# Performance work log

Measured on AMD Instinct MI355X. Metric: run time of the kernel, lower is better.

The kernel has to match this reference:

```python
import jax, jax.numpy as jnp
import numpy as np

EPS = 1e-5
INV_SQRT2 = 0.7071067811865476

def _rmsnorm(x, w):
    rms = jnp.sqrt(jnp.sum(x * x, axis=-1) / x.shape[-1] + EPS)
    return x / rms[..., None] * w

def _gelu(x):
    # exact erf-based GELU as in the torch module
    return x * (1.0 + jax.scipy.special.erf(x * INV_SQRT2)) * 0.5

def setup_inputs() -> dict:
    key = jax.random.key(0)
    ks = jax.random.split(key, 8)
    B, S, D, DFF = 4, 2048, 1024, 4096
    s = 0.02  # realistic init scale keeps softmax non-degenerate
    return {
        "x": jax.random.normal(ks[0], (B, S, D), jnp.float32),
        "ln1": jax.random.uniform(ks[1], (D,), jnp.float32),
        "ln2": jax.random.uniform(ks[2], (D,), jnp.float32),
        "ffn1": jax.random.normal(ks[3], (DFF, D), jnp.float32) * s,
        "ffn2": jax.random.normal(ks[4], (D, DFF), jnp.float32) * s,
        "k_proj": jax.random.normal(ks[5], (D, D), jnp.float32) * s,
        "q_proj": jax.random.normal(ks[6], (D, D), jnp.float32) * s,
        "v_proj": jax.random.normal(ks[7], (D, D), jnp.float32) * s,
        "out_proj": jax.random.normal(jax.random.fold_in(key, 99), (D, D), jnp.float32) * s,
    }

def reference(x, ln1, ln2, ffn1, ffn2, k_proj, q_proj, v_proj, out_proj):
    S = x.shape[1]
    d_k = x.shape[-1]
    # --- attention branch (single-head, as in source) ---
    h = _rmsnorm(x, ln1)
    Q = h @ q_proj.T  # [B,S,D]
    K = h @ k_proj.T
    V = h @ v_proj.T
    scores = jnp.einsum('bqd,bkd->bqk', Q, K) / jnp.sqrt(jnp.float32(d_k))
    attn = jax.nn.softmax(scores, axis=-1)
    # source: softmax first, then zero out strict-upper (future) entries, renormalize
    causal = jnp.tril(jnp.ones((S, S), jnp.float32))
    attn = attn * causal
    attn = attn / jnp.sum(attn, axis=-1, keepdims=True)
    mh = jnp.einsum('bqk,bkd->bqd', attn, V) @ out_proj
    y = x + mh
    # --- FFN branch: NOTE source feeds RMSNorm2(x), not y ---
    h2 = _rmsnorm(x, ln2)
    ff = _gelu(h2 @ ffn1.T) @ ffn2.T
    return y + ff
```

## Files before the change

kernel.cpp:

```cpp
#include <hip/hip_runtime.h>
#include <math.h>

typedef __bf16 bf16_t;
typedef __bf16 bf16x8 __attribute__((ext_vector_type(8)));
typedef float f32x4 __attribute__((ext_vector_type(4)));

#define LDS16(g, l) __builtin_amdgcn_global_load_lds( \
    (__attribute__((address_space(1))) void*)(g),     \
    (__attribute__((address_space(3))) void*)(l), 16, 0, 0)

__global__ __launch_bounds__(256) void cvt_all_kernel(
    const float* __restrict__ qp, const float* __restrict__ kp,
    const float* __restrict__ vp, const float* __restrict__ f1,
    const float* __restrict__ f2, bf16_t* __restrict__ qkvb,
    bf16_t* __restrict__ f1b, bf16_t* __restrict__ f2b)
{
    size_t i = ((size_t)blockIdx.x * 256 + threadIdx.x) * 4;
    const float* src;
    bf16_t* dst;
    if (i < 3145728) {
        if (i < 1048576)      { src = qp + i;            dst = qkvb + i; }
        else if (i < 2097152) { src = kp + (i - 1048576); dst = qkvb + i; }
        else                  { src = vp + (i - 2097152); dst = qkvb + i; }
    } else if (i < 7340032) { src = f1 + (i - 3145728); dst = f1b + (i - 3145728); }
    else                    { src = f2 + (i - 7340032); dst = f2b + (i - 7340032); }
    float4 v = *(const float4*)src;
    dst[0] = (bf16_t)v.x; dst[1] = (bf16_t)v.y;
    dst[2] = (bf16_t)v.z; dst[3] = (bf16_t)v.w;
}

__global__ __launch_bounds__(256) void transpose_cvt_kernel(
    const float* __restrict__ in, bf16_t* __restrict__ out, int rows, int cols)
{
    __shared__ float tile[32][33];
    int c0 = blockIdx.x * 32, r0 = blockIdx.y * 32;
    int tx = threadIdx.x & 31, ty = threadIdx.x >> 5;
#pragma unroll
    for (int i = 0; i < 32; i += 8)
        tile[ty + i][tx] = in[(size_t)(r0 + ty + i) * cols + c0 + tx];
    __syncthreads();
#pragma unroll
    for (int i = 0; i < 32; i += 8)
        out[(size_t)(c0 + ty + i) * rows + r0 + tx] = (bf16_t)tile[tx][ty + i];
}

__global__ __launch_bounds__(256) void transpose_bf16(
    const bf16_t* __restrict__ in, bf16_t* __restrict__ out,
    int rows, int ldin, long long sIn, long long sOut)
{
    __shared__ bf16_t tile[32][33];
    int b = blockIdx.z;
    const bf16_t* ip = in + (long long)b * sIn;
    bf16_t* op = out + (long long)b * sOut;
    int c0 = blockIdx.x * 32, r0 = blockIdx.y * 32;
    int tx = threadIdx.x & 31, ty = threadIdx.x >> 5;
#pragma unroll
    for (int i = 0; i < 32; i += 8)
        tile[ty + i][tx] = ip[(size_t)(r0 + ty + i) * ldin + c0 + tx];
    __syncthreads();
#pragma unroll
    for (int i = 0; i < 32; i += 8)
        op[(size_t)(c0 + ty + i) * rows + r0 + tx] = tile[tx][ty + i];
}

__global__ __launch_bounds__(256) void rmsnorm_kernel(
    const float* __restrict__ x, const float* __restrict__ w,
    bf16_t* __restrict__ h)
{
    int row = blockIdx.x;
    int t = threadIdx.x;
    float4 xv = ((const float4*)(x + (size_t)row * 1024))[t];
    float ss = xv.x * xv.x + xv.y * xv.y + xv.z * xv.z + xv.w * xv.w;
#pragma unroll
    for (int o = 32; o > 0; o >>= 1) ss += __shfl_xor(ss, o, 64);
    __shared__ float red[4];
    if ((t & 63) == 0) red[t >> 6] = ss;
    __syncthreads();
    ss = red[0] + red[1] + red[2] + red[3];
    float rinv = rsqrtf(ss * (1.0f / 1024.0f) + 1e-5f);
    float4 wv = ((const float4*)w)[t];
    bf16_t* hp = h + (size_t)row * 1024 + t * 4;
    hp[0] = (bf16_t)(xv.x * rinv * wv.x);
    hp[1] = (bf16_t)(xv.y * rinv * wv.y);
    hp[2] = (bf16_t)(xv.z * rinv * wv.z);
    hp[3] = (bf16_t)(xv.w * rinv * wv.w);
}

__global__ __launch_bounds__(256) void causal_softmax_kernel(bf16_t* __restrict__ SP)
{
    const int S = 2048;
    int q = blockIdx.x, b = blockIdx.y;
    bf16_t* row = SP + ((size_t)b * S + q) * S;
    int t = threadIdx.x;
    float v[8];
    float mx = -1e30f;
#pragma unroll
    for (int i = 0; i < 8; i++) {
        int j = i * 256 + t;
        v[i] = (j <= q) ? (float)row[j] : -1e30f;
        mx = fmaxf(mx, v[i]);
    }
#pragma unroll
    for (int o = 32; o > 0; o >>= 1) mx = fmaxf(mx, __shfl_xor(mx, o, 64));
    __shared__ float sm[4];
    if ((t & 63) == 0) sm[t >> 6] = mx;
    __syncthreads();
    mx = fmaxf(fmaxf(sm[0], sm[1]), fmaxf(sm[2], sm[3]));
    float e[8];
    float sum = 0.f;
#pragma unroll
    for (int i = 0; i < 8; i++) {
        e[i] = (v[i] > -1e29f) ? expf(v[i] - mx) : 0.f;
        sum += e[i];
    }
#pragma unroll
    for (int o = 32; o > 0; o >>= 1) sum += __shfl_xor(sum, o, 64);
    __shared__ float ssum[4];
    if ((t & 63) == 0) ssum[t >> 6] = sum;
    __syncthreads();
    sum = ssum[0] + ssum[1] + ssum[2] + ssum[3];
    float r = 1.0f / sum;
#pragma unroll
    for (int i = 0; i < 8; i++)
        row[i * 256 + t] = (bf16_t)(e[i] * r);
}

template <int EPI, bool CSKIP, bool CKLOOP>
__global__ __launch_bounds__(256) void gemm_bt(
    const bf16_t* __restrict__ A, int lda, const bf16_t* __restrict__ B, int ldb,
    void* Cv, int ldc, const float* R,
    int K, int Mt, long long sA, long long sB, long long sC, float scale)
{
    int id = blockIdx.x, bz = blockIdx.z;
    int xcd = id & 7, p = id >> 3;
    int chunk = Mt >> 3;
    int bm = xcd * chunk + (p % chunk);
    int bn = p / chunk;
    if (CSKIP && bn > bm) return;

    __shared__ __align__(16) bf16_t At[128 * 32];
    __shared__ __align__(16) bf16_t Bt[128 * 32];
    int t = threadIdx.x;
    int w = t >> 6, l = t & 63;
    int wm = w >> 1, wn = w & 1;
    int lane_m = l & 15, quad = l >> 4;

    const bf16_t* Ag = A + (long long)bz * sA + (size_t)(bm * 128) * lda;
    const bf16_t* Bg = B + (long long)bz * sB + (size_t)(bn * 128) * ldb;

    int Keff = K;
    if (CKLOOP) {
        int kk = (bm + 1) * 128;
        if (kk < K) Keff = kk;
    }

    f32x4 acc[4][4] = {};

    int r0 = w * 16 + (l >> 2);
    int g0 = ((l & 3) ^ ((l >> 3) & 3)) * 8;
    int r1 = r0 + 64;
    const bf16_t* a0 = Ag + (size_t)r0 * lda + g0;
    const bf16_t* a1 = Ag + (size_t)r1 * lda + g0;
    const bf16_t* b0 = Bg + (size_t)r0 * ldb + g0;
    const bf16_t* b1 = Bg + (size_t)r1 * ldb + g0;

    int sa = (quad ^ ((lane_m >> 1) & 3)) * 8;

    for (int kt = 0; kt < Keff; kt += 32) {
        __syncthreads();
        LDS16(a0 + kt, At + (size_t)w * 512);
        LDS16(a1 + kt, At + (size_t)(4 + w) * 512);
        LDS16(b0 + kt, Bt + (size_t)w * 512);
        LDS16(b1 + kt, Bt + (size_t)(4 + w) * 512);
        __syncthreads();

        bf16x8 af[4], bfr[4];
#pragma unroll
        for (int mi = 0; mi < 4; mi++)
            af[mi] = *(const bf16x8*)(At + (wm * 64 + mi * 16 + lane_m) * 32 + sa);
#pragma unroll
        for (int ni = 0; ni < 4; ni++)
            bfr[ni] = *(const bf16x8*)(Bt + (wn * 64 + ni * 16 + lane_m) * 32 + sa);
#pragma unroll
        for (int mi = 0; mi < 4; mi++)
#pragma unroll
            for (int ni = 0; ni < 4; ni++)
                acc[mi][ni] = __builtin_amdgcn_mfma_f32_16x16x32_bf16(
                    af[mi], bfr[ni], acc[mi][ni], 0, 0, 0);
    }

    long long cbase = (long long)bz * sC;
#pragma unroll
    for (int mi = 0; mi < 4; mi++) {
#pragma unroll
        for (int r = 0; r < 4; r++) {
            int row = bm * 128 + wm * 64 + mi * 16 + quad * 4 + r;
#pragma unroll
            for (int ni = 0; ni < 4; ni++) {
                int col = bn * 128 + wn * 64 + ni * 16 + lane_m;
                float v = acc[mi][ni][r];
                size_t idx = (size_t)(cbase + (long long)row * ldc + col);
                if (EPI == 0) {
                    ((bf16_t*)Cv)[idx] = (bf16_t)(v * scale);
                } else if (EPI == 1) {
                    float g = 0.5f * v * (1.0f + erff(v * 0.70710678118654752f));
                    ((bf16_t*)Cv)[idx] = (bf16_t)g;
                } else {
                    float rv = R[(size_t)row * ldc + col];
                    ((float*)Cv)[idx] = v + rv;
                }
            }
        }
    }
}

extern "C" void kernel_launch(void* const* d_in, const int* in_sizes, int n_in,
                              void* d_out, int out_size, void* d_ws, size_t ws_size,
                              hipStream_t stream)
{
    (void)in_sizes; (void)n_in; (void)out_size; (void)ws_size;
    const float* x    = (const float*)d_in[0];
    const float* ln1  = (const float*)d_in[1];
    const float* ln2  = (const float*)d_in[2];
    const float* ffn1 = (const float*)d_in[3];
    const float* ffn2 = (const float*)d_in[4];
    const float* kp   = (const float*)d_in[5];
    const float* qp   = (const float*)d_in[6];
    const float* vp   = (const float*)d_in[7];
    const float* op   = (const float*)d_in[8];
    float* out = (float*)d_out;

    const size_t MiB = 1048576;
    char* ws = (char*)d_ws;
    bf16_t* qkvb = (bf16_t*)(ws + 0 * MiB);
    bf16_t* opT  = (bf16_t*)(ws + 6 * MiB);
    bf16_t* f1b  = (bf16_t*)(ws + 8 * MiB);
    bf16_t* f2b  = (bf16_t*)(ws + 16 * MiB);
    bf16_t* h1   = (bf16_t*)(ws + 24 * MiB);
    bf16_t* VT   = (bf16_t*)(ws + 24 * MiB);
    bf16_t* h2   = (bf16_t*)(ws + 24 * MiB);
    bf16_t* QKVb = (bf16_t*)(ws + 40 * MiB);
    bf16_t* AV   = (bf16_t*)(ws + 40 * MiB);
    bf16_t* G    = (bf16_t*)(ws + 40 * MiB);
    bf16_t* SP   = (bf16_t*)d_out;

    dim3 blk(256);

    cvt_all_kernel<<<dim3(11264), blk, 0, stream>>>(
        qp, kp, vp, ffn1, ffn2, qkvb, f1b, f2b);
    transpose_cvt_kernel<<<dim3(32, 32), blk, 0, stream>>>(op, opT, 1024, 1024);

    rmsnorm_kernel<<<dim3(8192), blk, 0, stream>>>(x, ln1, h1);

    gemm_bt<0, false, false><<<dim3(1536), blk, 0, stream>>>(
        h1, 1024, qkvb, 1024, QKVb, 3072, nullptr, 1024, 64, 0, 0, 0, 1.0f);

    gemm_bt<0, true, false><<<dim3(256, 1, 4), blk, 0, stream>>>(
        QKVb, 3072, QKVb + 1024, 3072, SP, 2048, nullptr, 1024, 16,
        (long long)2048 * 3072, (long long)2048 * 3072, (long long)2048 * 2048,
        1.0f / 32.0f);

    transpose_bf16<<<dim3(32, 64, 4), blk, 0, stream>>>(
        QKVb + 2048, VT, 2048, 3072, (long long)2048 * 3072, (long long)1024 * 2048);

    causal_softmax_kernel<<<dim3(2048, 4), blk, 0, stream>>>(SP);

    gemm_bt<0, false, true><<<dim3(128, 1, 4), blk, 0, stream>>>(
        SP, 2048, VT, 2048, AV, 1024, nullptr, 2048, 16,
        (long long)2048 * 2048, (long long)1024 * 2048, (long long)2048 * 1024,
        1.0f);

    gemm_bt<2, false, false><<<dim3(512), blk, 0, stream>>>(
        AV, 1024, opT, 1024, out, 1024, x, 1024, 64, 0, 0, 0, 1.0f);

    rmsnorm_kernel<<<dim3(8192), blk, 0, stream>>>(x, ln2, h2);

    for (int half = 0; half < 2; half++) {
        gemm_bt<1, false, false><<<dim3(1024), blk, 0, stream>>>(
            h2, 1024, f1b + (size_t)half * 2048 * 1024, 1024, G, 2048, nullptr,
            1024, 64, 0, 0, 0, 1.0f);
        gemm_bt<2, false, false><<<dim3(512), blk, 0, stream>>>(
            G, 2048, f2b + half * 2048, 4096, out, 1024, out,
            2048, 64, 0, 0, 0, 1.0f);
    }
}
```

Before: 636.5 us.

## Double GEMM K-tile, fuse prep kernels, vectorize softmax, split-A FFN2 GEMM

The GEMM K step grows from 32 to 64, with a wider XOR swizzle. This halves the number of barrier pairs per K, at the cost of doubling LDS usage per block. The weight conversion, out_proj transpose and first RMSNorm are merged into one prep kernel to cut launch count. Causal softmax now uses 8-element vector loads and stores and only writes the columns up to the 128-aligned causal bound. When the workspace is big enough, the FFN runs as two FFN1 GEMMs plus a single FFN2 GEMM with K=4096 reading from two buffers, which avoids a second read-modify-write pass over the output.

After: 544.0 us. 1.17x faster.

```diff
diff --git a/kernel.cpp b/kernel.cpp
--- a/kernel.cpp
+++ b/kernel.cpp
@@ -9,58 +9,60 @@
     (__attribute__((address_space(1))) void*)(g),     \
     (__attribute__((address_space(3))) void*)(l), 16, 0, 0)
 
-__global__ __launch_bounds__(256) void cvt_all_kernel(
+__global__ __launch_bounds__(256) void prep_kernel(
     const float* __restrict__ qp, const float* __restrict__ kp,
     const float* __restrict__ vp, const float* __restrict__ f1,
-    const float* __restrict__ f2, bf16_t* __restrict__ qkvb,
-    bf16_t* __restrict__ f1b, bf16_t* __restrict__ f2b)
-{
-    size_t i = ((size_t)blockIdx.x * 256 + threadIdx.x) * 4;
-    const float* src;
-    bf16_t* dst;
-    if (i < 3145728) {
-        if (i < 1048576)      { src = qp + i;            dst = qkvb + i; }
-        else if (i < 2097152) { src = kp + (i - 1048576); dst = qkvb + i; }
-        else                  { src = vp + (i - 2097152); dst = qkvb + i; }
-    } else if (i < 7340032) { src = f1 + (i - 3145728); dst = f1b + (i - 3145728); }
-    else                    { src = f2 + (i - 7340032); dst = f2b + (i - 7340032); }
-    float4 v = *(const float4*)src;
-    dst[0] = (bf16_t)v.x; dst[1] = (bf16_t)v.y;
-    dst[2] = (bf16_t)v.z; dst[3] = (bf16_t)v.w;
-}
-
-__global__ __launch_bounds__(256) void transpose_cvt_kernel(
-    const float* __restrict__ in, bf16_t* __restrict__ out, int rows, int cols)
+    const float* __restrict__ f2, const float* __restrict__ op,
+    const float* __restrict__ x, const float* __restrict__ ln1,
+    bf16_t* __restrict__ qkvb, bf16_t* __restrict__ f1b,
+    bf16_t* __restrict__ f2b, bf16_t* __restrict__ opT,
+    bf16_t* __restrict__ h1)
 {
     __shared__ float tile[32][33];
-    int c0 = blockIdx.x * 32, r0 = blockIdx.y * 32;
-    int tx = threadIdx.x & 31, ty = threadIdx.x >> 5;
-#pragma unroll
-    for (int i = 0; i < 32; i += 8)
-        tile[ty + i][tx] = in[(size_t)(r0 + ty + i) * cols + c0 + tx];
-    __syncthreads();
-#pragma unroll
-    for (int i = 0; i < 32; i += 8)
-        out[(size_t)(c0 + ty + i) * rows + r0 + tx] = (bf16_t)tile[tx][ty + i];
-}
-
-__global__ __launch_bounds__(256) void transpose_bf16(
-    const bf16_t* __restrict__ in, bf16_t* __restrict__ out,
-    int rows, int ldin, long long sIn, long long sOut)
-{
-    __shared__ bf16_t tile[32][33];
-    int b = blockIdx.z;
-    const bf16_t* ip = in + (long long)b * sIn;
-    bf16_t* op = out + (long long)b * sOut;
-    int c0 = blockIdx.x * 32, r0 = blockIdx.y * 32;
-    int tx = threadIdx.x & 31, ty = threadIdx.x >> 5;
-#pragma unroll
-    for (int i = 0; i < 32; i += 8)
-        tile[ty + i][tx] = ip[(size_t)(r0 + ty + i) * ldin + c0 + tx];
-    __syncthreads();
-#pragma unroll
-    for (int i = 0; i < 32; i += 8)
-        op[(size_t)(c0 + ty + i) * rows + r0 + tx] = tile[tx][ty + i];
+    __shared__ float red[4];
+    int bid = blockIdx.x;
+    int t = threadIdx.x;
+    if (bid < 11264) {
+        size_t i = ((size_t)bid * 256 + t) * 4;
+        const float* src;
+        bf16_t* dst;
+        if (i < 3145728) {
+            if (i < 1048576)      { src = qp + i;             dst = qkvb + i; }
+            else if (i < 2097152) { src = kp + (i - 1048576); dst = qkvb + i; }
+            else                  { src = vp + (i - 2097152); dst = qkvb + i; }
+        } else if (i < 7340032) { src = f1 + (i - 3145728); dst = f1b + (i - 3145728); }
+        else                    { src = f2 + (i - 7340032); dst = f2b + (i - 7340032); }
+        float4 v = *(const float4*)src;
+        dst[0] = (bf16_t)v.x; dst[1] = (bf16_t)v.y;
+        dst[2] = (bf16_t)v.z; dst[3] = (bf16_t)v.w;
+    } else if (bid < 12288) {
+        int b2 = bid - 11264;
+        int c0 = (b2 & 31) * 32, r0 = (b2 >> 5) * 32;
+        int tx = t & 31, ty = t >> 5;
+#pragma unroll
+        for (int i = 0; i < 32; i += 8)
+            tile[ty + i][tx] = op[(size_t)(r0 + ty + i) * 1024 + c0 + tx];
+        __syncthreads();
+#pragma unroll
+        for (int i = 0; i < 32; i += 8)
+            opT[(size_t)(c0 + ty + i) * 1024 + r0 + tx] = (bf16_t)tile[tx][ty + i];
+    } else {
+        int row = bid - 12288;
+        float4 xv = ((const float4*)(x + (size_t)row * 1024))[t];
+        float ss = xv.x * xv.x + xv.y * xv.y + xv.z * xv.z + xv.w * xv.w;
+#pragma unroll
+        for (int o = 32; o > 0; o >>= 1) ss += __shfl_xor(ss, o, 64);
+        if ((t & 63) == 0) red[t >> 6] = ss;
+        __syncthreads();
+        ss = red[0] + red[1] + red[2] + red[3];
+        float rinv = rsqrtf(ss * (1.0f / 1024.0f) + 1e-5f);
+        float4 wv = ((const float4*)ln1)[t];
+        bf16_t* hp = h1 + (size_t)row * 1024 + t * 4;
+        hp[0] = (bf16_t)(xv.x * rinv * wv.x);
+        hp[1] = (bf16_t)(xv.y * rinv * wv.y);
+        hp[2] = (bf16_t)(xv.z * rinv * wv.z);
+        hp[3] = (bf16_t)(xv.w * rinv * wv.w);
+    }
 }
 
 __global__ __launch_bounds__(256) void rmsnorm_kernel(
@@ -86,26 +88,58 @@
     hp[3] = (bf16_t)(xv.w * rinv * wv.w);
 }
 
+__global__ __launch_bounds__(256) void transpose_bf16(
+    const bf16_t* __restrict__ in, bf16_t* __restrict__ out,
+    int rows, int ldin, long long sIn, long long sOut)
+{
+    __shared__ bf16_t tile[32][33];
+    int b = blockIdx.z;
+    const bf16_t* ip = in + (long long)b * sIn;
+    bf16_t* op = out + (long long)b * sOut;
+    int c0 = blockIdx.x * 32, r0 = blockIdx.y * 32;
+    int tx = threadIdx.x & 31, ty = threadIdx.x >> 5;
+#pragma unroll
+    for (int i = 0; i < 32; i += 8)
+        tile[ty + i][tx] = ip[(size_t)(r0 + ty + i) * ldin + c0 + tx];
+    __syncthreads();
+#pragma unroll
+    for (int i = 0; i < 32; i += 8)
+        op[(size_t)(c0 + ty + i) * rows + r0 + tx] = tile[tx][ty + i];
+}
+
 __global__ __launch_bounds__(256) void causal_softmax_kernel(bf16_t* __restrict__ SP)
 {
     const int S = 2048;
     int q = blockIdx.x, b = blockIdx.y;
     bf16_t* row = SP + ((size_t)b * S + q) * S;
     int t = threadIdx.x;
+    int j0 = t * 8;
+    int Jstore = ((q >> 7) + 1) << 7;
+
     float v[8];
-    float mx = -1e30f;
-#pragma unroll
-    for (int i = 0; i < 8; i++) {
-        int j = i * 256 + t;
-        v[i] = (j <= q) ? (float)row[j] : -1e30f;
-        mx = fmaxf(mx, v[i]);
-    }
+    if (j0 + 7 <= q) {
+        bf16x8 xv = *(const bf16x8*)(row + j0);
+#pragma unroll
+        for (int i = 0; i < 8; i++) v[i] = (float)xv[i];
+    } else if (j0 <= q) {
+#pragma unroll
+        for (int i = 0; i < 8; i++)
+            v[i] = (j0 + i <= q) ? (float)row[j0 + i] : -1e30f;
+    } else {
+#pragma unroll
+        for (int i = 0; i < 8; i++) v[i] = -1e30f;
+    }
+
+    float mx = v[0];
+#pragma unroll
+    for (int i = 1; i < 8; i++) mx = fmaxf(mx, v[i]);
 #pragma unroll
     for (int o = 32; o > 0; o >>= 1) mx = fmaxf(mx, __shfl_xor(mx, o, 64));
-    __shared__ float sm[4];
+    __shared__ float sm[4], ssum[4];
     if ((t & 63) == 0) sm[t >> 6] = mx;
     __syncthreads();
     mx = fmaxf(fmaxf(sm[0], sm[1]), fmaxf(sm[2], sm[3]));
+
     float e[8];
     float sum = 0.f;
 #pragma unroll
@@ -115,21 +149,26 @@
     }
 #pragma unroll
     for (int o = 32; o > 0; o >>= 1) sum += __shfl_xor(sum, o, 64);
-    __shared__ float ssum[4];
     if ((t & 63) == 0) ssum[t >> 6] = sum;
     __syncthreads();
     sum = ssum[0] + ssum[1] + ssum[2] + ssum[3];
     float r = 1.0f / sum;
-#pragma unroll
-    for (int i = 0; i < 8; i++)
-        row[i * 256 + t] = (bf16_t)(e[i] * r);
-}
-
-template <int EPI, bool CSKIP, bool CKLOOP>
+
+    if (j0 < Jstore) {
+        bf16x8 ov;
+#pragma unroll
+        for (int i = 0; i < 8; i++) ov[i] = (bf16_t)(e[i] * r);
+        *(bf16x8*)(row + j0) = ov;
+    }
+}
+
+template <int EPI, bool CSKIP, bool CKLOOP, bool ASPLIT>
 __global__ __launch_bounds__(256) void gemm_bt(
-    const bf16_t* __restrict__ A, int lda, const bf16_t* __restrict__ B, int ldb,
+    const bf16_t* __restrict__ A, const bf16_t* __restrict__ A2, int lda,
+    const bf16_t* __restrict__ B, int ldb,
     void* Cv, int ldc, const float* R,
-    int K, int Mt, long long sA, long long sB, long long sC, float scale)
+    int K, int Ksp, int Mt, long long sA, long long sB, long long sC,
+    float scale)
 {
     int id = blockIdx.x, bz = blockIdx.z;
     int xcd = id & 7, p = id >> 3;
@@ -138,8 +177,8 @@
     int bn = p / chunk;
     if (CSKIP && bn > bm) return;
 
-    __shared__ __align__(16) bf16_t At[128 * 32];
-    __shared__ __align__(16) bf16_t Bt[128 * 32];
+    __shared__ __align__(16) bf16_t At[128 * 64];
+    __shared__ __align__(16) bf16_t Bt[128 * 64];
     int t = threadIdx.x;
     int w = t >> 6, l = t & 63;
     int wm = w >> 1, wn = w & 1;
@@ -156,37 +195,51 @@
 
     f32x4 acc[4][4] = {};
 
-    int r0 = w * 16 + (l >> 2);
-    int g0 = ((l & 3) ^ ((l >> 3) & 3)) * 8;
-    int r1 = r0 + 64;
-    const bf16_t* a0 = Ag + (size_t)r0 * lda + g0;
-    const bf16_t* a1 = Ag + (size_t)r1 * lda + g0;
-    const bf16_t* b0 = Bg + (size_t)r0 * ldb + g0;
-    const bf16_t* b1 = Bg + (size_t)r1 * ldb + g0;
-
-    int sa = (quad ^ ((lane_m >> 1) & 3)) * 8;
-
-    for (int kt = 0; kt < Keff; kt += 32) {
+    int rb = w * 8 + (l >> 3);
+    int g0 = ((l & 7) ^ ((l >> 3) & 7)) * 8;
+    const bf16_t* a0[4];
+    const bf16_t* a1[4];
+    const bf16_t* b0[4];
+#pragma unroll
+    for (int j = 0; j < 4; j++) {
+        size_t ro = (size_t)(rb + 32 * j);
+        a0[j] = Ag + ro * lda + g0;
+        if (ASPLIT) a1[j] = A2 + (long long)bz * sA + (size_t)(bm * 128) * lda
+                           + ro * lda + g0;
+        b0[j] = Bg + ro * ldb + g0;
+    }
+
+    int s0 = (quad ^ (lane_m & 7)) * 8;
+    int s1 = ((4 + quad) ^ (lane_m & 7)) * 8;
+
+    for (int kt = 0; kt < Keff; kt += 64) {
         __syncthreads();
-        LDS16(a0 + kt, At + (size_t)w * 512);
-        LDS16(a1 + kt, At + (size_t)(4 + w) * 512);
-        LDS16(b0 + kt, Bt + (size_t)w * 512);
-        LDS16(b1 + kt, Bt + (size_t)(4 + w) * 512);
+#pragma unroll
+        for (int j = 0; j < 4; j++) {
+            const bf16_t* pa = a0[j] + kt;
+            if (ASPLIT && kt >= Ksp) pa = a1[j] + (kt - Ksp);
+            LDS16(pa, At + (size_t)w * 512 + j * 2048);
+            LDS16(b0[j] + kt, Bt + (size_t)w * 512 + j * 2048);
+        }
         __syncthreads();
 
-        bf16x8 af[4], bfr[4];
-#pragma unroll
-        for (int mi = 0; mi < 4; mi++)
-            af[mi] = *(const bf16x8*)(At + (wm * 64 + mi * 16 + lane_m) * 32 + sa);
-#pragma unroll
-        for (int ni = 0; ni < 4; ni++)
-            bfr[ni] = *(const bf16x8*)(Bt + (wn * 64 + ni * 16 + lane_m) * 32 + sa);
-#pragma unroll
-        for (int mi = 0; mi < 4; mi++)
+#pragma unroll
+        for (int h = 0; h < 2; h++) {
+            int sh = h ? s1 : s0;
+            bf16x8 af[4], bfr[4];
+#pragma unroll
+            for (int mi = 0; mi < 4; mi++)
+                af[mi] = *(const bf16x8*)(At + (wm * 64 + mi * 16 + lane_m) * 64 + sh);
 #pragma unroll
             for (int ni = 0; ni < 4; ni++)
-                acc[mi][ni] = __builtin_amdgcn_mfma_f32_16x16x32_bf16(
-                    af[mi], bfr[ni], acc[mi][ni], 0, 0, 0);
+                bfr[ni] = *(const bf16x8*)(Bt + (wn * 64 + ni * 16 + lane_m) * 64 + sh);
+#pragma unroll
+            for (int mi = 0; mi < 4; mi++)
+#pragma unroll
+                for (int ni = 0; ni < 4; ni++)
+                    acc[mi][ni] = __builtin_amdgcn_mfma_f32_16x16x32_bf16(
+                        af[mi], bfr[ni], acc[mi][ni], 0, 0, 0);
+        }
     }
 
     long long cbase = (long long)bz * sC;
@@ -218,7 +271,7 @@
                               void* d_out, int out_size, void* d_ws, size_t ws_size,
                               hipStream_t stream)
 {
-    (void)in_sizes; (void)n_in; (void)out_size; (void)ws_size;
+    (void)in_sizes; (void)n_in; (void)out_size;
     const float* x    = (const float*)d_in[0];
     const float* ln1  = (const float*)d_in[1];
     const float* ln2  = (const float*)d_in[2];
@@ -241,46 +294,63 @@
     bf16_t* h2   = (bf16_t*)(ws + 24 * MiB);
     bf16_t* QKVb = (bf16_t*)(ws + 40 * MiB);
     bf16_t* AV   = (bf16_t*)(ws + 40 * MiB);
-    bf16_t* G    = (bf16_t*)(ws + 40 * MiB);
+    bf16_t* G0   = (bf16_t*)(ws + 40 * MiB);
+    bf16_t* G1   = (bf16_t*)(ws + 72 * MiB);
     bf16_t* SP   = (bf16_t*)d_out;
+    bool bigws = ws_size >= 104 * MiB;
 
     dim3 blk(256);
-
-    cvt_all_kernel<<<dim3(11264), blk, 0, stream>>>(
-        qp, kp, vp, ffn1, ffn2, qkvb, f1b, f2b);
-    transpose_cvt_kernel<<<dim3(32, 32), blk, 0, stream>>>(op, opT, 1024, 1024);
-
-    rmsnorm_kernel<<<dim3(8192), blk, 0, stream>>>(x, ln1, h1);
-
-    gemm_bt<0, false, false><<<dim3(1536), blk, 0, stream>>>(
-        h1, 1024, qkvb, 1024, QKVb, 3072, nullptr, 1024, 64, 0, 0, 0, 1.0f);
-
-    gemm_bt<0, true, false><<<dim3(256, 1, 4), blk, 0, stream>>>(
-        QKVb, 3072, QKVb + 1024, 3072, SP, 2048, nullptr, 1024, 16,
+    const int HUGE_K = 1 << 30;
+
+    prep_kernel<<<dim3(20480), blk, 0, stream>>>(
+        qp, kp, vp, ffn1, ffn2, op, x, ln1, qkvb, f1b, f2b, opT, h1);
+
+    gemm_bt<0, false, false, false><<<dim3(1536), blk, 0, stream>>>(
+        h1, h1, 1024, qkvb, 1024, QKVb, 3072, nullptr,
+        1024, HUGE_K, 64, 0, 0, 0, 1.0f);
+
+    gemm_bt<0, true, false, false><<<dim3(256, 1, 4), blk, 0, stream>>>(
+        QKVb, QKVb, 3072, QKVb + 1024, 3072, SP, 2048, nullptr,
+        1024, HUGE_K, 16,
         (long long)2048 * 3072, (long long)2048 * 3072, (long long)2048 * 2048,
         1.0f / 32.0f);
 
     transpose_bf16<<<dim3(32, 64, 4), blk, 0, stream>>>(
-        QKVb + 2048, VT, 2048, 3072, (long long)2048 * 3072, (long long)1024 * 2048);
+        QKVb + 2048, VT, 2048, 3072,
+        (long long)2048 * 3072, (long long)1024 * 2048);
 
     causal_softmax_kernel<<<dim3(2048, 4), blk, 0, stream>>>(SP);
 
-    gemm_bt<0, false, true><<<dim3(128, 1, 4), blk, 0, stream>>>(
-        SP, 2048, VT, 2048, AV, 1024, nullptr, 2048, 16,
+    gemm_bt<0, false, true, false><<<dim3(128, 1, 4), blk, 0, stream>>>(
+        SP, SP, 2048, VT, 2048, AV, 1024, nullptr,
+        2048, HUGE_K, 16,
         (long long)2048 * 2048, (long long)1024 * 2048, (long long)2048 * 1024,
         1.0f);
 
-    gemm_bt<2, false, false><<<dim3(512), blk, 0, stream>>>(
-        AV, 1024, opT, 1024, out, 1024, x, 1024, 64, 0, 0, 0, 1.0f);
+    gemm_bt<2, false, false, false><<<dim3(512), blk, 0, stream>>>(
+        AV, AV, 1024, opT, 1024, out, 1024, x,
+        1024, HUGE_K, 64, 0, 0, 0, 1.0f);
 
     rmsnorm_kernel<<<dim3(8192), blk, 0, stream>>>(x, ln2, h2);
 
-    for (int half = 0; half < 2; half++) {
-        gemm_bt<1, false, false><<<dim3(1024), blk, 0, stream>>>(
-            h2, 1024, f1b + (size_t)half * 2048 * 1024, 1024, G, 2048, nullptr,
-            1024, 64, 0, 0, 0, 1.0f);
-        gemm_bt<2, false, false><<<dim3(512), blk, 0, stream>>>(
-            G, 2048, f2b + half * 2048, 4096, out, 1024, out,
-            2048, 64, 0, 0, 0, 1.0f);
-    }
-}
+    if (bigws) {
+        gemm_bt<1, false, false, false><<<dim3(1024), blk, 0, stream>>>(
+            h2, h2, 1024, f1b, 1024, G0, 2048, nullptr,
+            1024, HUGE_K, 64, 0, 0, 0, 1.0f);
+        gemm_bt<1, false, false, false><<<dim3(1024), blk, 0, stream>>>(
+            h2, h2, 1024, f1b + (size_t)2048 * 1024, 1024, G1, 2048, nullptr,
+            1024, HUGE_K, 64, 0, 0, 0, 1.0f);
+        gemm_bt<2, false, false, true><<<dim3(512), blk, 0, stream>>>(
+            G0, G1, 2048, f2b, 4096, out, 1024, out,
+            4096, 2048, 64, 0, 0, 0, 1.0f);
+    } else {
+        for (int half = 0; half < 2; half++) {
+            gemm_bt<1, false, false, false><<<dim3(1024), blk, 0, stream>>>(
+                h2, h2, 1024, f1b + (size_t)half * 2048 * 1024, 1024, G0, 2048,
+                nullptr, 1024, HUGE_K, 64, 0, 0, 0, 1.0f);
+            gemm_bt<2, false, false, false><<<dim3(512), blk, 0, stream>>>(
+                G0, G0, 2048, f2b + half * 2048, 4096, out, 1024, out,
+                2048, HUGE_K, 64, 0, 0, 0, 1.0f);
+        }
+    }
+}
```
